# Kernel tuning notes

Measured on AMD Instinct MI355X. Metric: run time of the kernel, lower is better.

## Reference

```python
import jax, jax.numpy as jnp
import numpy as np

# MoE config (matches init_kwargs)
DMODEL = 1024
N_EXPERTS = 32
EXPERT_SIZE = 512
N_HEADS = 4  # top-k experts per token
WEIGHT_SCALE = 1.0


def setup_inputs() -> dict:
    key = jax.random.key(0)
    k0, k1, k2, k3 = jax.random.split(key, 4)
    x = jax.random.normal(k0, (2, 2048, DMODEL), dtype=jnp.float32)
    # expert selection keys: [n_experts, dmodel], std = dmodel**-0.5
    expert_sel = jax.random.normal(k1, (N_EXPERTS, DMODEL), dtype=jnp.float32) * (DMODEL ** -0.5)
    # expert input keys: [n_experts, dmodel, expert_size], std = dmodel**-0.5
    keys = jax.random.normal(k2, (N_EXPERTS, DMODEL, EXPERT_SIZE), dtype=jnp.float32) * (DMODEL ** -0.5)
    # expert output values: [n_experts, expert_size, v_dim], std = (n_experts*expert_size)**-0.5
    values = jax.random.normal(k3, (N_EXPERTS, EXPERT_SIZE, DMODEL), dtype=jnp.float32) * ((N_EXPERTS * EXPERT_SIZE) ** -0.5)
    return {"x": x, "expert_sel": expert_sel, "keys": keys, "values": values}


def reference(x, expert_sel, keys, values):
    # x: [B, S, D]
    B, S, D = x.shape
    xt = x.reshape(-1, D)                      # [N, D] tokens
    N = xt.shape[0]

    # --- routing: sigmoid gating + top-k expert selection ---
    sel_logits = jnp.einsum('nd,ed->ne', xt, expert_sel)   # [N, E]
    gates = jax.nn.sigmoid(sel_logits)                     # [N, E]
    sel_val, sel_idx = jax.lax.top_k(gates, N_HEADS)       # [N, K]

    # scatter selected gate values into a dense [N, E] gate matrix
    # (zero gate for non-selected experts == gather/scatter of expert MLPs)
    gate_full = jnp.zeros_like(gates).at[jnp.arange(N)[:, None], sel_idx].set(sel_val)

    # --- expert MLP: key scores -> ReLU -> gate-weighted -> value combine ---
    scores = jax.nn.relu(jnp.einsum('nd,edf->nef', xt, keys))   # [N, E, F]
    scores = scores * gate_full[:, :, None]                     # mask + sigmoid gate
    out = jnp.einsum('nef,efv->nv', scores, values)             # [N, V]

    return out.reshape(B, S, -1)
```

## Files before the change

### kernel.cpp

```cpp
#include <hip/hip_runtime.h>

#define DMODEL 1024
#define NEXP   32
#define FDIM   512
#define TOPK   4

#define MT    128
#define NT    128
#define BK    64
#define RTB   8
#define NBORD 64

using short8 = __attribute__((ext_vector_type(8))) short;
using f32x4  = __attribute__((ext_vector_type(4))) float;

#define AS1 __attribute__((address_space(1)))
#define AS3 __attribute__((address_space(3)))
__device__ __forceinline__ void gload_lds16(const void* g, void* l) {
    __builtin_amdgcn_global_load_lds((const AS1 unsigned int*)g, (AS3 unsigned int*)l, 16, 0, 0);
}

__device__ __forceinline__ unsigned short f2b(float f) {
    unsigned int u = __float_as_uint(f);
    unsigned int r = (u + 0x7FFFu + ((u >> 16) & 1u)) >> 16;
    return (unsigned short)r;
}
__device__ __forceinline__ float b2f(unsigned short u) {
    return __uint_as_float((unsigned int)u << 16);
}

__global__ __launch_bounds__(256) void route_a(
    const float* __restrict__ x, const float* __restrict__ esel,
    unsigned short* __restrict__ xb,
    unsigned int* __restrict__ sel_e, float* __restrict__ sel_g, int ntok)
{
    int tile0 = blockIdx.x * RTB;
    int tid = threadIdx.x;

    __shared__ float xs[RTB][DMODEL];
    __shared__ float gs[RTB][NEXP];

    {
        const float4* src = (const float4*)(x + (size_t)tile0 * DMODEL);
        float4* dst = (float4*)&xs[0][0];
        int navail = min(RTB, ntok - tile0) * (DMODEL / 4);
        for (int i = tid; i < RTB * (DMODEL / 4); i += 256)
            dst[i] = src[i < navail ? i : 0];
    }
    __syncthreads();

    int e = tid >> 3, sub = tid & 7;
    float4 acc0 = {0,0,0,0}, acc1 = {0,0,0,0}, acc2 = {0,0,0,0}, acc3 = {0,0,0,0};
    float4 acc4 = {0,0,0,0}, acc5 = {0,0,0,0}, acc6 = {0,0,0,0}, acc7 = {0,0,0,0};
    const float* er = esel + (size_t)e * DMODEL + sub * 4;
    #pragma unroll 4
    for (int j = 0; j < DMODEL / 32; j++) {
        float4 ev = *(const float4*)(er + j * 32);
        int kk = sub * 4 + j * 32;
        float4 x0 = *(const float4*)(&xs[0][kk]);
        float4 x1 = *(const float4*)(&xs[1][kk]);
        float4 x2 = *(const float4*)(&xs[2][kk]);
        float4 x3 = *(const float4*)(&xs[3][kk]);
        float4 x4 = *(const float4*)(&xs[4][kk]);
        float4 x5 = *(const float4*)(&xs[5][kk]);
        float4 x6 = *(const float4*)(&xs[6][kk]);
        float4 x7 = *(const float4*)(&xs[7][kk]);
        acc0.x += ev.x*x0.x; acc0.y += ev.y*x0.y; acc0.z += ev.z*x0.z; acc0.w += ev.w*x0.w;
        acc1.x += ev.x*x1.x; acc1.y += ev.y*x1.y; acc1.z += ev.z*x1.z; acc1.w += ev.w*x1.w;
        acc2.x += ev.x*x2.x; acc2.y += ev.y*x2.y; acc2.z += ev.z*x2.z; acc2.w += ev.w*x2.w;
        acc3.x += ev.x*x3.x; acc3.y += ev.y*x3.y; acc3.z += ev.z*x3.z; acc3.w += ev.w*x3.w;
        acc4.x += ev.x*x4.x; acc4.y += ev.y*x4.y; acc4.z += ev.z*x4.z; acc4.w += ev.w*x4.w;
        acc5.x += ev.x*x5.x; acc5.y += ev.y*x5.y; acc5.z += ev.z*x5.z; acc5.w += ev.w*x5.w;
        acc6.x += ev.x*x6.x; acc6.y += ev.y*x6.y; acc6.z += ev.z*x6.z; acc6.w += ev.w*x6.w;
        acc7.x += ev.x*x7.x; acc7.y += ev.y*x7.y; acc7.z += ev.z*x7.z; acc7.w += ev.w*x7.w;
    }
    {
        float s[RTB] = {
            acc0.x+acc0.y+acc0.z+acc0.w, acc1.x+acc1.y+acc1.z+acc1.w,
            acc2.x+acc2.y+acc2.z+acc2.w, acc3.x+acc3.y+acc3.z+acc3.w,
            acc4.x+acc4.y+acc4.z+acc4.w, acc5.x+acc5.y+acc5.z+acc5.w,
            acc6.x+acc6.y+acc6.z+acc6.w, acc7.x+acc7.y+acc7.z+acc7.w };
        #pragma unroll
        for (int t = 0; t < RTB; t++) {
            float v = s[t];
            v += __shfl_xor(v, 1);
            v += __shfl_xor(v, 2);
            v += __shfl_xor(v, 4);
            if (sub == 0) gs[t][e] = 1.f / (1.f + expf(-v));
        }
    }
    __syncthreads();

    {
        int t = tid >> 5, e2 = tid & 31;
        int tok = tile0 + t;
        if (tok < ntok) {
            float v = gs[t][e2];
            #pragma unroll
            for (int r = 0; r < TOPK; r++) {
                float bv = v; int bi = e2;
                #pragma unroll
                for (int sft = 16; sft >= 1; sft >>= 1) {
                    float ov = __shfl_xor(bv, sft, 32);
                    int   oi = __shfl_xor(bi, sft, 32);
                    if (ov > bv || (ov == bv && oi < bi)) { bv = ov; bi = oi; }
                }
                if (e2 == bi) v = -1e30f;
                if (e2 == r) {
                    sel_e[(size_t)tok * TOPK + r] = (unsigned)bi;
                    sel_g[(size_t)tok * TOPK + r] = bv;
                }
            }
        }
    }

    {
        int navail = min(RTB, ntok - tile0) * (DMODEL / 4);
        ushort4* dst = (ushort4*)(xb + (size_t)tile0 * DMODEL);
        const float4* srcl = (const float4*)&xs[0][0];
        for (int i = tid; i < navail; i += 256) {
            float4 v = srcl[i];
            ushort4 o;
            o.x = f2b(v.x); o.y = f2b(v.y); o.z = f2b(v.z); o.w = f2b(v.w);
            dst[i] = o;
        }
    }
}

__global__ __launch_bounds__(256) void hist_k(
    const unsigned int* __restrict__ sel_e, int* __restrict__ ghist, int nsel)
{
    __shared__ int h[NEXP];
    int tid = threadIdx.x;
    if (tid < NEXP) h[tid] = 0;
    __syncthreads();
    int chunk = (nsel + gridDim.x - 1) / gridDim.x;
    int i0 = blockIdx.x * chunk, i1 = min(i0 + chunk, nsel);
    for (int i = i0 + tid; i < i1; i += 256)
        atomicAdd(&h[sel_e[i]], 1);
    __syncthreads();
    if (tid < NEXP) ghist[blockIdx.x * NEXP + tid] = h[tid];
}

__global__ __launch_bounds__(64) void scan2_k(
    const int* __restrict__ ghist, int* __restrict__ goff,
    int* __restrict__ counts, int* __restrict__ base,
    int* __restrict__ tiles, int* __restrict__ ntiles, int nb)
{
    int e = threadIdx.x;
    if (e < NEXP) {
        int s = 0;
        for (int b = 0; b < nb; b++) {
            goff[b * NEXP + e] = s;
            s += ghist[b * NEXP + e];
        }
        counts[e] = s;
    }
    __syncthreads();
    if (e == 0) {
        int s = 0, nt = 0;
        for (int e2 = 0; e2 < NEXP; e2++) {
            base[e2] = s;
            int c = counts[e2];
            for (int t0 = 0; t0 < c; t0 += MT) tiles[nt++] = (e2 << 8) | (t0 / MT);
            s += c;
        }
        *ntiles = nt;
    }
}

__global__ __launch_bounds__(256) void scat_k(
    const unsigned int* __restrict__ sel_e, const float* __restrict__ sel_g,
    const int* __restrict__ goff,
    int* __restrict__ tok_list, float* __restrict__ gate_list,
    unsigned int* __restrict__ slotinfo, int nsel, int ntok)
{
    __shared__ int c[NEXP];
    int tid = threadIdx.x;
    if (tid < NEXP) c[tid] = goff[blockIdx.x * NEXP + tid];
    __syncthreads();
    int chunk = (nsel + gridDim.x - 1) / gridDim.x;
    int i0 = blockIdx.x * chunk, i1 = min(i0 + chunk, nsel);
    for (int i = i0 + tid; i < i1; i += 256) {
        unsigned int e = sel_e[i];
        float g = sel_g[i];
        int pos = atomicAdd(&c[e], 1);
        tok_list [(size_t)e * ntok + pos] = i >> 2;
        gate_list[(size_t)e * ntok + pos] = g;
        slotinfo[i] = (e << 16) | (unsigned)pos;
    }
}

__global__ __launch_bounds__(256) void prep_t(const float* __restrict__ src,
                                              unsigned short* __restrict__ dst,
                                              int R, int C) {
    __shared__ float tile[64][65];
    int e  = blockIdx.z;
    int r0 = blockIdx.y * 64, c0 = blockIdx.x * 64;
    const float* s = src + (size_t)e * R * C;
    unsigned short* d = dst + (size_t)e * R * C;
    for (int i = 0; i < 16; i++) {
        int c = i * 256 + threadIdx.x;
        int rr = c >> 6, cc = c & 63;
        tile[rr][cc] = s[(size_t)(r0 + rr) * C + c0 + cc];
    }
    __syncthreads();
    for (int i = 0; i < 16; i++) {
        int c = i * 256 + threadIdx.x;
        int wr = c >> 6, wc = c & 63;
        d[(size_t)(c0 + wr) * R + r0 + wc] = f2b(tile[wc][wr]);
    }
}

__global__ __launch_bounds__(256) void gemm1_k(
    const unsigned short* __restrict__ xb,
    const unsigned short* __restrict__ kt,
    const int* __restrict__ counts, const int* __restrict__ base,
    const int* __restrict__ tiles, const int* __restrict__ ntiles,
    const int* __restrict__ tok_list, const float* __restrict__ gate_list,
    unsigned short* __restrict__ hs, int ntok)
{
    int ti = blockIdx.x;
    if (ti >= *ntiles) return;
    int code = tiles[ti];
    int e = code >> 8, t0 = (code & 255) * MT;
    int cnt  = counts[e];
    int f0   = blockIdx.y * NT;
    int live = min(MT, cnt - t0);

    __shared__ unsigned short Xs[MT * BK];
    __shared__ unsigned short Ks[NT * BK];
    __shared__ int   toks[MT];
    __shared__ float gts[MT];

    int tid = threadIdx.x, lane = tid & 63, w = tid >> 6;
    int lr = lane & 15, lg = lane >> 4;

    if (tid < MT) {
        bool lv = tid < live;
        toks[tid] = lv ? tok_list [(size_t)e * ntok + t0 + tid] : 0;
        gts[tid]  = lv ? gate_list[(size_t)e * ntok + t0 + tid] : 0.f;
    }
    __syncthreads();

    int lrow = lane >> 3;
    int scol = ((lane & 7) ^ lrow) * 8;
    const unsigned short* ke = kt + (size_t)e * FDIM * DMODEL + (size_t)f0 * DMODEL;
    const unsigned short* sx[4];
    const unsigned short* sk[4];
    unsigned short* dx[4];
    unsigned short* dk[4];
    #pragma unroll
    for (int j = 0; j < 4; j++) {
        int ch = 4 * w + j;
        int row = ch * 8 + lrow;
        sx[j] = xb + (size_t)toks[row] * DMODEL + scol;
        sk[j] = ke + (size_t)row * DMODEL + scol;
        dx[j] = Xs + ch * 512;
        dk[j] = Ks + ch * 512;
    }

    f32x4 acc[8][2];
    #pragma unroll
    for (int m = 0; m < 8; m++)
        #pragma unroll
        for (int n = 0; n < 2; n++)
            acc[m][n] = (f32x4){0.f, 0.f, 0.f, 0.f};

    for (int k0 = 0; k0 < DMODEL; k0 += BK) {
        #pragma unroll
        for (int j = 0; j < 4; j++) {
            gload_lds16(sx[j] + k0, dx[j]);
            gload_lds16(sk[j] + k0, dk[j]);
        }
        __syncthreads();
        #pragma unroll
        for (int ks = 0; ks < 2; ks++) {
            short8 a[8];
            #pragma unroll
            for (int m = 0; m < 8; m++) {
                int row = m * 16 + lr;
                a[m] = *(const short8*)(Xs + row * BK + (((ks * 4 + lg) ^ (lr & 7)) * 8));
            }
            #pragma unroll
            for (int n = 0; n < 2; n++) {
                int row = w * 32 + n * 16 + lr;
                short8 b = *(const short8*)(Ks + row * BK + (((ks * 4 + lg) ^ (lr & 7)) * 8));
                #pragma unroll
                for (int m = 0; m < 8; m++)
                    acc[m][n] = __builtin_amdgcn_mfma_f32_16x16x32_bf16(a[m], b, acc[m][n], 0, 0, 0);
            }
        }
        __syncthreads();
    }

    int hb = base[e] + t0;
    #pragma unroll
    for (int m = 0; m < 8; m++) {
        #pragma unroll
        for (int n = 0; n < 2; n++) {
            int col = f0 + w * 32 + n * 16 + lr;
            #pragma unroll
            for (int r = 0; r < 4; r++) {
                int row = m * 16 + lg * 4 + r;
                if (row < live)
                    hs[(size_t)(hb + row) * FDIM + col] = f2b(fmaxf(acc[m][n][r], 0.f) * gts[row]);
            }
        }
    }
}

__global__ __launch_bounds__(256) void gemm2_k(
    const unsigned short* __restrict__ hs,
    const unsigned short* __restrict__ vt,
    const int* __restrict__ counts, const int* __restrict__ base,
    const int* __restrict__ tiles, const int* __restrict__ ntiles,
    unsigned short* __restrict__ ys)
{
    int ti = blockIdx.x;
    if (ti >= *ntiles) return;
    int code = tiles[ti];
    int e = code >> 8, t0 = (code & 255) * MT;
    int cnt  = counts[e];
    int v0   = blockIdx.y * NT;
    int live = min(MT, cnt - t0);
    int hb   = base[e] + t0;

    __shared__ unsigned short Hs[MT * BK];
    __shared__ unsigned short Vs[NT * BK];

    int tid = threadIdx.x, lane = tid & 63, w = tid >> 6;
    int lr = lane & 15, lg = lane >> 4;

    int lrow = lane >> 3;
    int scol = ((lane & 7) ^ lrow) * 8;
    const unsigned short* he = hs + (size_t)hb * FDIM;
    const unsigned short* ve = vt + (size_t)e * DMODEL * FDIM + (size_t)v0 * FDIM;
    const unsigned short* sh[4];
    const unsigned short* sv[4];
    unsigned short* dh[4];
    unsigned short* dv[4];
    #pragma unroll
    for (int j = 0; j < 4; j++) {
        int ch = 4 * w + j;
        int row = ch * 8 + lrow;
        sh[j] = he + (size_t)row * FDIM + scol;
        sv[j] = ve + (size_t)row * FDIM + scol;
        dh[j] = Hs + ch * 512;
        dv[j] = Vs + ch * 512;
    }

    f32x4 acc[8][2];
    #pragma unroll
    for (int m = 0; m < 8; m++)
        #pragma unroll
        for (int n = 0; n < 2; n++)
            acc[m][n] = (f32x4){0.f, 0.f, 0.f, 0.f};

    for (int k0 = 0; k0 < FDIM; k0 += BK) {
        #pragma unroll
        for (int j = 0; j < 4; j++) {
            gload_lds16(sh[j] + k0, dh[j]);
            gload_lds16(sv[j] + k0, dv[j]);
        }
        __syncthreads();
        #pragma unroll
        for (int ks = 0; ks < 2; ks++) {
            short8 a[8];
            #pragma unroll
            for (int m = 0; m < 8; m++) {
                int row = m * 16 + lr;
                a[m] = *(const short8*)(Hs + row * BK + (((ks * 4 + lg) ^ (lr & 7)) * 8));
            }
            #pragma unroll
            for (int n = 0; n < 2; n++) {
                int row = w * 32 + n * 16 + lr;
                short8 b = *(const short8*)(Vs + row * BK + (((ks * 4 + lg) ^ (lr & 7)) * 8));
                #pragma unroll
                for (int m = 0; m < 8; m++)
                    acc[m][n] = __builtin_amdgcn_mfma_f32_16x16x32_bf16(a[m], b, acc[m][n], 0, 0, 0);
            }
        }
        __syncthreads();
    }

    #pragma unroll
    for (int m = 0; m < 8; m++) {
        #pragma unroll
        for (int n = 0; n < 2; n++) {
            int col = v0 + w * 32 + n * 16 + lr;
            #pragma unroll
            for (int r = 0; r < 4; r++) {
                int row = m * 16 + lg * 4 + r;
                if (row < live)
                    ys[(size_t)(hb + row) * DMODEL + col] = f2b(acc[m][n][r]);
            }
        }
    }
}

__global__ __launch_bounds__(256) void combine_k(
    const unsigned short* __restrict__ ys, const unsigned int* __restrict__ slotinfo,
    const int* __restrict__ base, float* __restrict__ out)
{
    int tok = blockIdx.x;
    unsigned int s0 = slotinfo[(size_t)tok * TOPK + 0];
    unsigned int s1 = slotinfo[(size_t)tok * TOPK + 1];
    unsigned int s2 = slotinfo[(size_t)tok * TOPK + 2];
    unsigned int s3 = slotinfo[(size_t)tok * TOPK + 3];
    const ushort4* y0 = (const ushort4*)(ys + (size_t)(base[s0 >> 16] + (s0 & 0xFFFF)) * DMODEL);
    const ushort4* y1 = (const ushort4*)(ys + (size_t)(base[s1 >> 16] + (s1 & 0xFFFF)) * DMODEL);
    const ushort4* y2 = (const ushort4*)(ys + (size_t)(base[s2 >> 16] + (s2 & 0xFFFF)) * DMODEL);
    const ushort4* y3 = (const ushort4*)(ys + (size_t)(base[s3 >> 16] + (s3 & 0xFFFF)) * DMODEL);
    int i = threadIdx.x;
    ushort4 a = y0[i], b = y1[i], c = y2[i], d = y3[i];
    float4 o;
    o.x = b2f(a.x) + b2f(b.x) + b2f(c.x) + b2f(d.x);
    o.y = b2f(a.y) + b2f(b.y) + b2f(c.y) + b2f(d.y);
    o.z = b2f(a.z) + b2f(b.z) + b2f(c.z) + b2f(d.z);
    o.w = b2f(a.w) + b2f(b.w) + b2f(c.w) + b2f(d.w);
    ((float4*)(out + (size_t)tok * DMODEL))[i] = o;
}

#define BTF 16
__global__ __launch_bounds__(256) void expert_k(
    const float* __restrict__ x, const float* __restrict__ keys,
    const float* __restrict__ values, const int* __restrict__ counts,
    const int* __restrict__ tok_list, const float* __restrict__ gate_list,
    float* __restrict__ out, int ntok)
{
    int e   = blockIdx.y;
    int cnt = counts[e];
    int t0  = blockIdx.x * BTF;
    if (t0 >= cnt) return;
    int nt = (cnt - t0 < BTF) ? (cnt - t0) : BTF;

    __shared__ float xs[BTF][DMODEL];
    __shared__ float hsl[BTF][FDIM];
    __shared__ int   toks[BTF];
    __shared__ float gts[BTF];

    if (threadIdx.x < BTF) {
        int t = threadIdx.x;
        bool live = (t < nt);
        toks[t] = live ? tok_list [(size_t)e * ntok + t0 + t] : 0;
        gts[t]  = live ? gate_list[(size_t)e * ntok + t0 + t] : 0.f;
    }
    __syncthreads();
    for (int i = threadIdx.x; i < BTF * (DMODEL / 4); i += 256) {
        int r = i >> 8, c = i & 255;
        ((float4*)xs[r])[c] = ((const float4*)(x + (size_t)toks[r] * DMODEL))[c];
    }
    __syncthreads();

    {
        int f = threadIdx.x * 2;
        float acc0[BTF], acc1[BTF];
        #pragma unroll
        for (int t = 0; t < BTF; t++) { acc0[t] = 0.f; acc1[t] = 0.f; }
        const float* kp = keys + (size_t)e * DMODEL * FDIM + f;
        for (int k = 0; k < DMODEL; k += 4) {
            const float* kr = kp + (size_t)k * FDIM;
            float2 kv0 = *(const float2*)(kr);
            float2 kv1 = *(const float2*)(kr + FDIM);
            float2 kv2 = *(const float2*)(kr + 2 * FDIM);
            float2 kv3 = *(const float2*)(kr + 3 * FDIM);
            #pragma unroll
            for (int t = 0; t < BTF; t++) {
                float4 xv = *(const float4*)(&xs[t][k]);
                acc0[t] += xv.x * kv0.x + xv.y * kv1.x + xv.z * kv2.x + xv.w * kv3.x;
                acc1[t] += xv.x * kv0.y + xv.y * kv1.y + xv.z * kv2.y + xv.w * kv3.y;
            }
        }
        #pragma unroll
        for (int t = 0; t < BTF; t++) {
            float g = gts[t];
            hsl[t][f]     = fmaxf(acc0[t], 0.f) * g;
            hsl[t][f + 1] = fmaxf(acc1[t], 0.f) * g;
        }
    }
    __syncthreads();

    {
        int v = threadIdx.x * 4;
        float acc[BTF][4];
        #pragma unroll
        for (int t = 0; t < BTF; t++) { acc[t][0]=0.f; acc[t][1]=0.f; acc[t][2]=0.f; acc[t][3]=0.f; }
        const float* vp = values + (size_t)e * FDIM * DMODEL + v;
        for (int k = 0; k < FDIM; k += 2) {
            float4 va0 = *(const float4*)(vp + (size_t)k * DMODEL);
            float4 va1 = *(const float4*)(vp + (size_t)(k + 1) * DMODEL);
            #pragma unroll
            for (int t = 0; t < BTF; t++) {
                float2 hv = *(const float2*)(&hsl[t][k]);
                acc[t][0] += hv.x * va0.x + hv.y * va1.x;
                acc[t][1] += hv.x * va0.y + hv.y * va1.y;
                acc[t][2] += hv.x * va0.z + hv.y * va1.z;
                acc[t][3] += hv.x * va0.w + hv.y * va1.w;
            }
        }
        #pragma unroll
        for (int t = 0; t < BTF; t++) {
            if (t < nt) {
                float* orow = out + (size_t)toks[t] * DMODEL + v;
                atomicAdd(orow + 0, acc[t][0]);
                atomicAdd(orow + 1, acc[t][1]);
                atomicAdd(orow + 2, acc[t][2]);
                atomicAdd(orow + 3, acc[t][3]);
            }
        }
    }
}

extern "C" void kernel_launch(void* const* d_in, const int* in_sizes, int n_in,
                              void* d_out, int out_size, void* d_ws, size_t ws_size,
                              hipStream_t stream) {
    const float* x      = (const float*)d_in[0];
    const float* esel   = (const float*)d_in[1];
    const float* keys   = (const float*)d_in[2];
    const float* values = (const float*)d_in[3];
    float* out = (float*)d_out;
    int ntok = in_sizes[0] / DMODEL;

    const size_t OFF_BASE = 512;
    const size_t OFF_NT   = 1024;
    const size_t OFF_TILE = 2048;
    const size_t OFF_HIST = 16 << 10;
    const size_t OFF_GOFF = 32 << 10;
    const size_t OFF_SLOT = 64 << 10;
    const size_t OFF_SELE = 128 << 10;
    const size_t OFF_SELG = 192 << 10;
    const size_t OFF_TOK  = 256 << 10;
    const size_t OFF_GATE = 1ull << 20;
    const size_t OFF_XB   = 2ull << 20;
    const size_t OFF_KT   = 12ull << 20;
    const size_t OFF_VT   = 46ull << 20;
    const size_t OFF_HS   = 80ull << 20;
    const size_t OFF_YS   = 98ull << 20;
    const size_t NEED     = OFF_YS + (size_t)ntok * TOPK * DMODEL * sizeof(float) + (1 << 20);

    int*      counts    = (int*)d_ws;
    int*      ebase     = (int*)((char*)d_ws + OFF_BASE);
    int*      ntiles    = (int*)((char*)d_ws + OFF_NT);
    int*      tiles     = (int*)((char*)d_ws + OFF_TILE);
    int*      ghist     = (int*)((char*)d_ws + OFF_HIST);
    int*      goff      = (int*)((char*)d_ws + OFF_GOFF);
    unsigned* slotinfo  = (unsigned*)((char*)d_ws + OFF_SLOT);
    unsigned* sel_e     = (unsigned*)((char*)d_ws + OFF_SELE);
    float*    sel_g     = (float*)((char*)d_ws + OFF_SELG);
    int*      tok_list  = (int*)((char*)d_ws + OFF_TOK);
    float*    gate_list = (float*)((char*)d_ws + OFF_GATE);
    unsigned short* xb  = (unsigned short*)((char*)d_ws + OFF_XB);

    int nsel = ntok * TOPK;
    int rblocks = (ntok + RTB - 1) / RTB;
    route_a<<<rblocks, 256, 0, stream>>>(x, esel, xb, sel_e, sel_g, ntok);
    hist_k<<<NBORD, 256, 0, stream>>>(sel_e, ghist, nsel);
    scan2_k<<<1, 64, 0, stream>>>(ghist, goff, counts, ebase, tiles, ntiles, NBORD);
    scat_k<<<NBORD, 256, 0, stream>>>(sel_e, sel_g, goff, tok_list, gate_list,
                                      slotinfo, nsel, ntok);

    if (ws_size >= NEED) {
        unsigned short* kt = (unsigned short*)((char*)d_ws + OFF_KT);
        unsigned short* vt = (unsigned short*)((char*)d_ws + OFF_VT);
        unsigned short* hs = (unsigned short*)((char*)d_ws + OFF_HS);
        unsigned short* ys = (unsigned short*)((char*)d_ws + OFF_YS);

        prep_t<<<dim3(FDIM / 64, DMODEL / 64, NEXP), 256, 0, stream>>>(keys,   kt, DMODEL, FDIM);
        prep_t<<<dim3(DMODEL / 64, FDIM / 64, NEXP), 256, 0, stream>>>(values, vt, FDIM, DMODEL);

        int maxt = (ntok * TOPK + MT - 1) / MT + NEXP;
        gemm1_k<<<dim3(maxt, FDIM / NT), 256, 0, stream>>>(
            xb, kt, counts, ebase, tiles, ntiles, tok_list, gate_list, hs, ntok);
        gemm2_k<<<dim3(maxt, DMODEL / NT), 256, 0, stream>>>(
            hs, vt, counts, ebase, tiles, ntiles, ys);
        combine_k<<<ntok, 256, 0, stream>>>(ys, slotinfo, ebase, out);
    } else {
        hipMemsetAsync(out, 0, (size_t)out_size * sizeof(float), stream);
        int ntiles2 = (ntok + BTF - 1) / BTF;
        expert_k<<<dim3(ntiles2, NEXP), 256, 0, stream>>>(
            x, keys, values, counts, tok_list, gate_list, out, ntok);
    }
}
```

Measured before the change: 196.5 us.

## Double-buffer LDS tiles in both expert GEMMs to overlap loads with MFMA

Both grouped GEMM kernels get two LDS buffers each for the A and B tiles. The first K-slice is loaded before the loop, and each iteration issues the async global-to-LDS loads for the next slice before running MFMAs on the current one. This is meant to hide global memory latency behind compute and drop one barrier per iteration. In exchange, LDS use per block doubles, which can lower occupancy. Correctness relies on the end-of-iteration barrier waiting for the outstanding async loads.

```diff
diff --git a/kernel.cpp b/kernel.cpp
--- a/kernel.cpp
+++ b/kernel.cpp
@@ -228,8 +228,8 @@
     int f0   = blockIdx.y * NT;
     int live = min(MT, cnt - t0);
 
-    __shared__ unsigned short Xs[MT * BK];
-    __shared__ unsigned short Ks[NT * BK];
+    __shared__ unsigned short Xs[2][MT * BK];
+    __shared__ unsigned short Ks[2][NT * BK];
     __shared__ int   toks[MT];
     __shared__ float gts[MT];
 
@@ -248,16 +248,14 @@
     const unsigned short* ke = kt + (size_t)e * FDIM * DMODEL + (size_t)f0 * DMODEL;
     const unsigned short* sx[4];
     const unsigned short* sk[4];
-    unsigned short* dx[4];
-    unsigned short* dk[4];
+    int dofs[4];
     #pragma unroll
     for (int j = 0; j < 4; j++) {
         int ch = 4 * w + j;
         int row = ch * 8 + lrow;
         sx[j] = xb + (size_t)toks[row] * DMODEL + scol;
         sk[j] = ke + (size_t)row * DMODEL + scol;
-        dx[j] = Xs + ch * 512;
-        dk[j] = Ks + ch * 512;
+        dofs[j] = ch * 512;
     }
 
     f32x4 acc[8][2];
@@ -267,31 +265,43 @@
         for (int n = 0; n < 2; n++)
             acc[m][n] = (f32x4){0.f, 0.f, 0.f, 0.f};
 
+    #pragma unroll
+    for (int j = 0; j < 4; j++) {
+        gload_lds16(sx[j], &Xs[0][dofs[j]]);
+        gload_lds16(sk[j], &Ks[0][dofs[j]]);
+    }
+    __syncthreads();
+
+    int cur = 0;
     for (int k0 = 0; k0 < DMODEL; k0 += BK) {
-        #pragma unroll
-        for (int j = 0; j < 4; j++) {
-            gload_lds16(sx[j] + k0, dx[j]);
-            gload_lds16(sk[j] + k0, dk[j]);
-        }
-        __syncthreads();
+        if (k0 + BK < DMODEL) {
+            #pragma unroll
+            for (int j = 0; j < 4; j++) {
+                gload_lds16(sx[j] + k0 + BK, &Xs[cur ^ 1][dofs[j]]);
+                gload_lds16(sk[j] + k0 + BK, &Ks[cur ^ 1][dofs[j]]);
+            }
+        }
+        const unsigned short* Xc = Xs[cur];
+        const unsigned short* Kc = Ks[cur];
         #pragma unroll
         for (int ks = 0; ks < 2; ks++) {
             short8 a[8];
             #pragma unroll
             for (int m = 0; m < 8; m++) {
                 int row = m * 16 + lr;
-                a[m] = *(const short8*)(Xs + row * BK + (((ks * 4 + lg) ^ (lr & 7)) * 8));
+                a[m] = *(const short8*)(Xc + row * BK + (((ks * 4 + lg) ^ (lr & 7)) * 8));
             }
             #pragma unroll
             for (int n = 0; n < 2; n++) {
                 int row = w * 32 + n * 16 + lr;
-                short8 b = *(const short8*)(Ks + row * BK + (((ks * 4 + lg) ^ (lr & 7)) * 8));
+                short8 b = *(const short8*)(Kc + row * BK + (((ks * 4 + lg) ^ (lr & 7)) * 8));
                 #pragma unroll
                 for (int m = 0; m < 8; m++)
                     acc[m][n] = __builtin_amdgcn_mfma_f32_16x16x32_bf16(a[m], b, acc[m][n], 0, 0, 0);
             }
         }
         __syncthreads();
+        cur ^= 1;
     }
 
     int hb = base[e] + t0;
@@ -326,8 +336,8 @@
     int live = min(MT, cnt - t0);
     int hb   = base[e] + t0;
 
-    __shared__ unsigned short Hs[MT * BK];
-    __shared__ unsigned short Vs[NT * BK];
+    __shared__ unsigned short Hs[2][MT * BK];
+    __shared__ unsigned short Vs[2][NT * BK];
 
     int tid = threadIdx.x, lane = tid & 63, w = tid >> 6;
     int lr = lane & 15, lg = lane >> 4;
@@ -338,16 +348,14 @@
     const unsigned short* ve = vt + (size_t)e * DMODEL * FDIM + (size_t)v0 * FDIM;
     const unsigned short* sh[4];
     const unsigned short* sv[4];
-    unsigned short* dh[4];
-    unsigned short* dv[4];
+    int dofs[4];
     #pragma unroll
     for (int j = 0; j < 4; j++) {
         int ch = 4 * w + j;
         int row = ch * 8 + lrow;
         sh[j] = he + (size_t)row * FDIM + scol;
         sv[j] = ve + (size_t)row * FDIM + scol;
-        dh[j] = Hs + ch * 512;
-        dv[j] = Vs + ch * 512;
+        dofs[j] = ch * 512;
     }
 
     f32x4 acc[8][2];
@@ -357,31 +365,43 @@
         for (int n = 0; n < 2; n++)
             acc[m][n] = (f32x4){0.f, 0.f, 0.f, 0.f};
 
+    #pragma unroll
+    for (int j = 0; j < 4; j++) {
+        gload_lds16(sh[j], &Hs[0][dofs[j]]);
+        gload_lds16(sv[j], &Vs[0][dofs[j]]);
+    }
+    __syncthreads();
+
+    int cur = 0;
     for (int k0 = 0; k0 < FDIM; k0 += BK) {
-        #pragma unroll
-        for (int j = 0; j < 4; j++) {
-            gload_lds16(sh[j] + k0, dh[j]);
-            gload_lds16(sv[j] + k0, dv[j]);
-        }
-        __syncthreads();
+        if (k0 + BK < FDIM) {
+            #pragma unroll
+            for (int j = 0; j < 4; j++) {
+                gload_lds16(sh[j] + k0 + BK, &Hs[cur ^ 1][dofs[j]]);
+                gload_lds16(sv[j] + k0 + BK, &Vs[cur ^ 1][dofs[j]]);
+            }
+        }
+        const unsigned short* Hc = Hs[cur];
+        const unsigned short* Vc = Vs[cur];
         #pragma unroll
         for (int ks = 0; ks < 2; ks++) {
             short8 a[8];
             #pragma unroll
             for (int m = 0; m < 8; m++) {
                 int row = m * 16 + lr;
-                a[m] = *(const short8*)(Hs + row * BK + (((ks * 4 + lg) ^ (lr & 7)) * 8));
+                a[m] = *(const short8*)(Hc + row * BK + (((ks * 4 + lg) ^ (lr & 7)) * 8));
             }
             #pragma unroll
             for (int n = 0; n < 2; n++) {
                 int row = w * 32 + n * 16 + lr;
-                short8 b = *(const short8*)(Vs + row * BK + (((ks * 4 + lg) ^ (lr & 7)) * 8));
+                short8 b = *(const short8*)(Vc + row * BK + (((ks * 4 + lg) ^ (lr & 7)) * 8));
                 #pragma unroll
                 for (int m = 0; m < 8; m++)
                     acc[m][n] = __builtin_amdgcn_mfma_f32_16x16x32_bf16(a[m], b, acc[m][n], 0, 0, 0);
             }
         }
         __syncthreads();
+        cur ^= 1;
     }
 
     #pragma unroll
```

Measured after the change: 201.3 us. +2.4%, slower.
